# Optimization experiments

Hardware: AMD Instinct MI355X
Metric: run time of the kernel (lower is better)

## Reference

```python
import jax, jax.numpy as jnp
import numpy as np

B, S, D, E, K = 4, 4096, 4096, 64, 2
TEMP = 1.0  # temperature=1.0 -> scale by 1/temperature kept for faithfulness


def setup_inputs() -> dict:
    key = jax.random.key(0)
    k1, k2 = jax.random.split(key)
    x = jax.random.normal(k1, (B, S, D), dtype=jnp.float32)
    W_gate = jax.random.normal(k2, (E, D), dtype=jnp.float32) * (D ** -0.5)
    return {"x": x, "W_gate": W_gate}


def reference(x, W_gate):
    # gate: Linear(d_model, n_experts, bias=False) -> logits [B,S,E]
    logits = jnp.einsum('bsd,ed->bse', x, W_gate)
    # temperature scaling (eval mode: no jitter / expert dropout / gumbel)
    logits = logits * (1.0 / TEMP)
    probs_full = jax.nn.softmax(logits, axis=-1)           # [B,S,E]
    topk_vals, idx = jax.lax.top_k(logits, K)              # [B,S,K]
    scores = jax.nn.softmax(topk_vals, axis=-1)            # renormalized top-k gates
    # z-loss: mean(logsumexp(logits)^2)
    z = jax.nn.logsumexp(logits, axis=-1)                  # [B,S]
    z_loss = jnp.mean(z * z)
    # aux stats (computed under no_grad in the original)
    importance = jax.lax.stop_gradient(jnp.mean(probs_full, axis=(0, 1)))  # [E]
    idx_flat = idx.reshape(-1)
    counts = jnp.zeros((E,), probs_full.dtype).at[idx_flat].add(1.0)       # [E]
    load = jax.lax.stop_gradient(counts / jnp.maximum(jnp.sum(counts), 1.0))
    return (idx, scores, probs_full, z_loss, importance, load)
```

## Files before the change

kernel.cpp:

```cpp
#include <hip/hip_runtime.h>

namespace {
constexpr int D = 4096;
constexpr int E = 64;
constexpr int M = 16384;
constexpr int BM = 32;
constexpr int BK = 64;
constexpr int NT = D / BK;
constexpr int NBLK = M / BM;

constexpr int OFF_IDX = 0;
constexpr int OFF_SCORES = 32768;
constexpr int OFF_PROBS = 65536;
constexpr int OFF_Z = 1114112;
constexpr int OFF_IMP = 1114113;
constexpr int OFF_LOAD = 1114177;

constexpr int WS_STRIDE = 132;
}

__device__ __forceinline__ void gload16(const float* g, float* l) {
  __builtin_amdgcn_global_load_lds(
      (const __attribute__((address_space(1))) void*)g,
      (__attribute__((address_space(3))) void*)l, 16, 0, 0);
}

__global__ __launch_bounds__(512, 4) void router_fused(
    const float* __restrict__ xg, const float* __restrict__ wg,
    float* __restrict__ out, float* __restrict__ ws) {
  __shared__ float smem[12288];

  const int t = threadIdx.x;
  const int u = t & 63;
  const int s = t >> 6;
  const int tx = u & 7;
  const int ty = u >> 3;
  const int r0 = blockIdx.x * BM;

  const float* srcp[3];
  int dstf[3];
#pragma unroll
  for (int j = 0; j < 3; ++j) {
    const int c = 3 * s + j;
    dstf[j] = c * 256;
    if (c < 8) {
      const int row = c * 4 + (u >> 4);
      srcp[j] = xg + (size_t)(r0 + row) * D + (((u & 15) ^ c) << 2);
    } else {
      const int row = (c - 8) * 4 + (u >> 4);
      srcp[j] = wg + (size_t)row * D + (((u & 15) ^ ((c - 8) >> 1)) << 2);
    }
  }
  auto stage = [&](int r, float* buf) {
    const int rk = r * BK;
#pragma unroll
    for (int j = 0; j < 3; ++j) gload16(srcp[j] + rk, buf + dstf[j]);
  };

  int xoff[2], woff[2];
#pragma unroll
  for (int kr = 0; kr < 2; ++kr) {
    const int kc = s * 2 + kr;
    xoff[kr] = ty * 256 + ((kc ^ ty) << 2);
    woff[kr] = 2048 + tx * 512 + ((kc ^ tx) << 2);
  }

  float acc[4][8];
#pragma unroll
  for (int i = 0; i < 4; ++i)
#pragma unroll
    for (int j = 0; j < 8; ++j) acc[i][j] = 0.f;

  stage(0, smem);

  for (int r = 0; r < NT; ++r) {
    __syncthreads();
    if (r + 1 < NT) stage(r + 1, smem + ((r + 1) & 1) * 6144);

    const float* buf = smem + (r & 1) * 6144;
#pragma unroll
    for (int kr = 0; kr < 2; ++kr) {
      float4 bw[8];
#pragma unroll
      for (int j = 0; j < 8; ++j)
        bw[j] = *(const float4*)&buf[woff[kr] + j * 64];
#pragma unroll
      for (int i = 0; i < 4; ++i) {
        const float4 ax = *(const float4*)&buf[xoff[kr] + i * 64];
#pragma unroll
        for (int j = 0; j < 8; ++j) {
          acc[i][j] = fmaf(ax.x, bw[j].x, acc[i][j]);
          acc[i][j] = fmaf(ax.y, bw[j].y, acc[i][j]);
          acc[i][j] = fmaf(ax.z, bw[j].z, acc[i][j]);
          acc[i][j] = fmaf(ax.w, bw[j].w, acc[i][j]);
        }
      }
    }
  }

  float v[8];
#pragma unroll
  for (int q = 0; q < 8; ++q) v[q] = 0.f;

#pragma unroll
  for (int ph = 0; ph < 2; ++ph) {
    __syncthreads();
    {
      float* P = smem;
      const int su2 = (s * 64 + u) * 2;
#pragma unroll
      for (int il = 0; il < 2; ++il)
#pragma unroll
        for (int jj = 0; jj < 4; ++jj)
          *(float2*)&P[(il * 4 + jj) * 1024 + su2] =
              make_float2(acc[ph * 2 + il][2 * jj],
                          acc[ph * 2 + il][2 * jj + 1]);
    }
    __syncthreads();
    if (s < 4 && (s >> 1) == ph) {
      const float* P = smem;
      const int base_p = (s & 1) * 4;
#pragma unroll
      for (int sl = 0; sl < 8; ++sl)
#pragma unroll
        for (int qq = 0; qq < 4; ++qq) {
          const float2 f =
              *(const float2*)&P[(base_p + qq) * 1024 + (sl * 64 + u) * 2];
          v[2 * qq] += f.x;
          v[2 * qq + 1] += f.y;
        }
    }
  }

  const int row = (u >> 3) * 4 + s;
  const int ebase = (u & 7) * 8;
  const int gr = r0 + row;

  __syncthreads();
  float* PW = smem;
  float* zw = smem + 256;
  int* cnt = (int*)(smem + 260);
  if (t < 64) cnt[t] = 0;
  __syncthreads();

  if (s < 4) {
    float v1 = v[0]; int i1 = ebase;
    float v2 = -3.402823466e+38f; int i2 = 0;
#pragma unroll
    for (int q = 1; q < 8; ++q) {
      const float x = v[q];
      if (x > v1) { v2 = v1; i2 = i1; v1 = x; i1 = ebase + q; }
      else if (x > v2) { v2 = x; i2 = ebase + q; }
    }
#pragma unroll
    for (int m = 1; m <= 4; m <<= 1) {
      const float o1 = __shfl_xor(v1, m);
      const int oi1 = __shfl_xor(i1, m);
      const float o2 = __shfl_xor(v2, m);
      const int oi2 = __shfl_xor(i2, m);
      if (o1 > v1 || (o1 == v1 && oi1 < i1)) {
        const bool c2 = (o2 > v1) || (o2 == v1 && oi2 < i1);
        v2 = c2 ? o2 : v1; i2 = c2 ? oi2 : i1;
        v1 = o1; i1 = oi1;
      } else if (o1 > v2 || (o1 == v2 && oi1 < i2)) {
        v2 = o1; i2 = oi1;
      }
    }

    float p[8];
    float ssum = 0.f;
#pragma unroll
    for (int q = 0; q < 8; ++q) { p[q] = __expf(v[q] - v1); ssum += p[q]; }
#pragma unroll
    for (int m = 1; m <= 4; m <<= 1) ssum += __shfl_xor(ssum, m);
    const float rs = 1.f / ssum;
#pragma unroll
    for (int q = 0; q < 8; ++q) p[q] *= rs;

    {
      const float4 o0 = {p[0], p[1], p[2], p[3]};
      const float4 o1 = {p[4], p[5], p[6], p[7]};
      *(float4*)&out[OFF_PROBS + (size_t)gr * 64 + ebase] = o0;
      *(float4*)&out[OFF_PROBS + (size_t)gr * 64 + ebase + 4] = o1;
    }
    const float z = v1 + __logf(ssum);
    const float z2 = z * z;

    if ((u & 7) == 0) {
      out[OFF_IDX + 2 * gr] = (float)i1;
      out[OFF_IDX + 2 * gr + 1] = (float)i2;
      const float e1 = __expf(v2 - v1);
      const float s0 = 1.f / (1.f + e1);
      out[OFF_SCORES + 2 * gr] = s0;
      out[OFF_SCORES + 2 * gr + 1] = e1 * s0;
      atomicAdd(&cnt[i1], 1);
      atomicAdd(&cnt[i2], 1);
    }

    float cs[8];
#pragma unroll
    for (int q = 0; q < 8; ++q) cs[q] = p[q];
#pragma unroll
    for (int m = 8; m <= 32; m <<= 1)
#pragma unroll
      for (int q = 0; q < 8; ++q) cs[q] += __shfl_xor(cs[q], m);
    float zs = z2;
#pragma unroll
    for (int m = 8; m <= 32; m <<= 1) zs += __shfl_xor(zs, m);
    if (u < 8) {
      const float4 c0 = {cs[0], cs[1], cs[2], cs[3]};
      const float4 c1 = {cs[4], cs[5], cs[6], cs[7]};
      *(float4*)&PW[s * 64 + u * 8] = c0;
      *(float4*)&PW[s * 64 + u * 8 + 4] = c1;
      if (u == 0) zw[s] = zs;
    }
  }
  __syncthreads();

  if (t < 64) {
    const float ic =
        PW[t] + PW[64 + t] + PW[128 + t] + PW[192 + t];
    ws[(size_t)blockIdx.x * WS_STRIDE + t] = ic;
    ws[(size_t)blockIdx.x * WS_STRIDE + 64 + t] = (float)cnt[t];
  } else if (t == 64) {
    ws[(size_t)blockIdx.x * WS_STRIDE + 128] = zw[0] + zw[1] + zw[2] + zw[3];
  }
}

__global__ __launch_bounds__(512) void router_reduce(
    const float* __restrict__ ws, float* __restrict__ out) {
  __shared__ float part[4][128];
  __shared__ float zp[4];
  const int t = threadIdx.x;
  const int c = t >> 7;
  const int slot = t & 127;
  float v = 0.f;
#pragma unroll 8
  for (int i = 0; i < 128; ++i)
    v += ws[(size_t)(c * 128 + i) * WS_STRIDE + slot];
  part[c][slot] = v;
  if (t < 4) {
    float zz = 0.f;
#pragma unroll 8
    for (int i = 0; i < 128; ++i)
      zz += ws[(size_t)(t * 128 + i) * WS_STRIDE + 128];
    zp[t] = zz;
  }
  __syncthreads();
  if (t < 128) {
    const float s4 = part[0][t] + part[1][t] + part[2][t] + part[3][t];
    if (t < 64)
      out[OFF_IMP + t] = s4 * (1.f / 16384.f);
    else
      out[OFF_LOAD + (t - 64)] = s4 * (1.f / 32768.f);
  } else if (t == 128) {
    out[OFF_Z] = (zp[0] + zp[1] + zp[2] + zp[3]) * (1.f / 16384.f);
  }
}

extern "C" void kernel_launch(void* const* d_in, const int* in_sizes, int n_in,
                              void* d_out, int out_size, void* d_ws, size_t ws_size,
                              hipStream_t stream) {
  const float* x = (const float*)d_in[0];
  const float* wgate = (const float*)d_in[1];
  float* out = (float*)d_out;
  float* ws = (float*)d_ws;

  router_fused<<<dim3(NBLK), dim3(512), 0, stream>>>(x, wgate, out, ws);
  router_reduce<<<dim3(1), dim3(512), 0, stream>>>(ws, out);
}
```

Measured before the change: 412.8 us.

## Pre-transpose gate weights into register-friendly layout and read them directly from global

A small pre-kernel rewrites W_gate into a tiled layout matching each thread's float4 access pattern. The main GEMM kernel then loads weight fragments straight from global/L2 into registers instead of staging them through LDS, so only x tiles go through shared memory. This cuts LDS traffic and footprint, which could raise occupancy, but it adds an extra launch and makes every block issue direct global loads for the weights.

```diff
diff --git a/kernel.cpp b/kernel.cpp
--- a/kernel.cpp
+++ b/kernel.cpp
@@ -17,6 +17,7 @@
 constexpr int OFF_LOAD = 1114177;
 
 constexpr int WS_STRIDE = 132;
+constexpr int WT_FLOATS = 262144;
 }
 
 __device__ __forceinline__ void gload16(const float* g, float* l) {
@@ -25,10 +26,36 @@
       (__attribute__((address_space(3))) void*)l, 16, 0, 0);
 }
 
+__global__ __launch_bounds__(256) void wt_build(const float* __restrict__ wg,
+                                                float* __restrict__ wt) {
+  __shared__ float ls[64][65];
+  const int b = blockIdx.x;
+  const int t = threadIdx.x;
+  const int e = t >> 2, c = t & 3;
+#pragma unroll
+  for (int i = 0; i < 4; ++i) {
+    const float4 v =
+        *(const float4*)(wg + (size_t)e * D + b * 64 + c * 4 + i * 16);
+    *(float4*)&ls[e][c * 4 + i * 16] = v;
+  }
+  __syncthreads();
+#pragma unroll
+  for (int i = 0; i < 4; ++i) {
+    const int idx = t * 4 + i * 1024;
+    const int kcl = idx >> 8;
+    const int rem = idx & 255;
+    const int j = rem >> 5;
+    const int tx = (rem >> 2) & 7;
+    const float* lr = &ls[tx * 8 + j][kcl * 4];
+    const float4 o = {lr[0], lr[1], lr[2], lr[3]};
+    *(float4*)(wt + (size_t)b * 4096 + idx) = o;
+  }
+}
+
 __global__ __launch_bounds__(512, 4) void router_fused(
-    const float* __restrict__ xg, const float* __restrict__ wg,
+    const float* __restrict__ xg, const float* __restrict__ wt,
     float* __restrict__ out, float* __restrict__ ws) {
-  __shared__ float smem[12288];
+  __shared__ float smem[8192];
 
   const int t = threadIdx.x;
   const int u = t & 63;
@@ -37,33 +64,19 @@
   const int ty = u >> 3;
   const int r0 = blockIdx.x * BM;
 
-  const float* srcp[3];
-  int dstf[3];
-#pragma unroll
-  for (int j = 0; j < 3; ++j) {
-    const int c = 3 * s + j;
-    dstf[j] = c * 256;
-    if (c < 8) {
-      const int row = c * 4 + (u >> 4);
-      srcp[j] = xg + (size_t)(r0 + row) * D + (((u & 15) ^ c) << 2);
-    } else {
-      const int row = (c - 8) * 4 + (u >> 4);
-      srcp[j] = wg + (size_t)row * D + (((u & 15) ^ ((c - 8) >> 1)) << 2);
-    }
-  }
-  auto stage = [&](int r, float* buf) {
-    const int rk = r * BK;
-#pragma unroll
-    for (int j = 0; j < 3; ++j) gload16(srcp[j] + rk, buf + dstf[j]);
-  };
-
-  int xoff[2], woff[2];
+  const float* srcX =
+      xg + (size_t)(r0 + s * 4 + (u >> 4)) * D + (((u & 15) ^ s) << 2);
+  const int dstf = s * 256;
+  auto stage = [&](int r, float* buf) { gload16(srcX + r * BK, buf + dstf); };
+
+  int xoff[2];
 #pragma unroll
   for (int kr = 0; kr < 2; ++kr) {
     const int kc = s * 2 + kr;
     xoff[kr] = ty * 256 + ((kc ^ ty) << 2);
-    woff[kr] = 2048 + tx * 512 + ((kc ^ tx) << 2);
-  }
+  }
+
+  const float* wtp = wt + (size_t)(s * 2) * 256 + tx * 4;
 
   float acc[4][8];
 #pragma unroll
@@ -75,15 +88,16 @@
 
   for (int r = 0; r < NT; ++r) {
     __syncthreads();
-    if (r + 1 < NT) stage(r + 1, smem + ((r + 1) & 1) * 6144);
-
-    const float* buf = smem + (r & 1) * 6144;
+    if (r + 1 < NT) stage(r + 1, smem + ((r + 1) & 1) * 2048);
+
+    const float* buf = smem + (r & 1) * 2048;
+    const float* wr_ = wtp + (size_t)r * 4096;
 #pragma unroll
     for (int kr = 0; kr < 2; ++kr) {
       float4 bw[8];
 #pragma unroll
       for (int j = 0; j < 8; ++j)
-        bw[j] = *(const float4*)&buf[woff[kr] + j * 64];
+        bw[j] = *(const float4*)(wr_ + kr * 256 + j * 32);
 #pragma unroll
       for (int i = 0; i < 4; ++i) {
         const float4 ax = *(const float4*)&buf[xoff[kr] + i * 64];
@@ -218,8 +232,7 @@
   __syncthreads();
 
   if (t < 64) {
-    const float ic =
-        PW[t] + PW[64 + t] + PW[128 + t] + PW[192 + t];
+    const float ic = PW[t] + PW[64 + t] + PW[128 + t] + PW[192 + t];
     ws[(size_t)blockIdx.x * WS_STRIDE + t] = ic;
     ws[(size_t)blockIdx.x * WS_STRIDE + 64 + t] = (float)cnt[t];
   } else if (t == 64) {
@@ -264,8 +277,10 @@
   const float* x = (const float*)d_in[0];
   const float* wgate = (const float*)d_in[1];
   float* out = (float*)d_out;
-  float* ws = (float*)d_ws;
-
-  router_fused<<<dim3(NBLK), dim3(512), 0, stream>>>(x, wgate, out, ws);
-  router_reduce<<<dim3(1), dim3(512), 0, stream>>>(ws, out);
-}
+  float* wt = (float*)d_ws;
+  float* stats = wt + WT_FLOATS;
+
+  wt_build<<<dim3(64), dim3(256), 0, stream>>>(wgate, wt);
+  router_fused<<<dim3(NBLK), dim3(512), 0, stream>>>(x, wt, out, stats);
+  router_reduce<<<dim3(1), dim3(512), 0, stream>>>(stats, out);
+}
```

Measured after the change: 523.8 us. 1.27x slower.
